# Optimization experiments

Hardware: AMD Instinct MI355X
Metric: run time of the kernel (lower is better)

The kernel has to match this reference:

```python
import jax, jax.numpy as jnp
import numpy as np

B, S, D, H = 16, 512, 1024, 16
DK = D // H
DFF = 4 * D
EPS = 1e-5
NEG = -1e9


def fake_quant(w):
    # EMA int8 symmetric per-tensor fake quantization of weights (inference view)
    scale = jnp.max(jnp.abs(w)) / 127.0
    wq = jnp.round(w / scale) * scale
    # straight-through estimator form (no-op in fwd)
    return w + jax.lax.stop_gradient(wq - w)


def layer_norm(x, g, b):
    mu = jnp.mean(x, axis=-1, keepdims=True)
    var = jnp.mean(jnp.square(x - mu), axis=-1, keepdims=True)
    return (x - mu) * jax.lax.rsqrt(var + EPS) * g + b


def setup_inputs() -> dict:
    key = jax.random.key(0)
    ks = jax.random.split(key, 16)
    std = 0.02
    inp = {
        'x': jax.random.normal(ks[0], (B, S, D), jnp.float32),
        'mask': jax.random.randint(ks[1], (B, 1, S, S), 0, 2, jnp.int32),
        'wq': jax.random.normal(ks[2], (D, D), jnp.float32) * std,
        'bq': jnp.zeros((D,), jnp.float32),
        'wk': jax.random.normal(ks[3], (D, D), jnp.float32) * std,
        'bk': jnp.zeros((D,), jnp.float32),
        'wv': jax.random.normal(ks[4], (D, D), jnp.float32) * std,
        'bv': jnp.zeros((D,), jnp.float32),
        'wo': jax.random.normal(ks[5], (D, D), jnp.float32) * std,
        'bo': jnp.zeros((D,), jnp.float32),
        'w1': jax.random.normal(ks[6], (D, DFF), jnp.float32) * std,
        'b1': jnp.zeros((DFF,), jnp.float32),
        'w2': jax.random.normal(ks[7], (DFF, D), jnp.float32) * std,
        'b2': jnp.zeros((D,), jnp.float32),
        'ln1_g': jnp.ones((D,), jnp.float32),
        'ln1_b': jnp.zeros((D,), jnp.float32),
        'ln2_g': jnp.ones((D,), jnp.float32),
        'ln2_b': jnp.zeros((D,), jnp.float32),
        'layer': 0,
    }
    return inp


def reference(x, mask, wq, bq, wk, bk, wv, bv, wo, bo, w1, b1, w2, b2,
              ln1_g, ln1_b, ln2_g, ln2_b, layer):
    # --- input sublayer: x + attention(LN(x)) (dropout = identity at eval) ---
    h = layer_norm(x, ln1_g, ln1_b)
    q = (h @ fake_quant(wq) + bq).reshape(B, S, H, DK).transpose(0, 2, 1, 3)
    k = (h @ fake_quant(wk) + bk).reshape(B, S, H, DK).transpose(0, 2, 1, 3)
    v = (h @ fake_quant(wv) + bv).reshape(B, S, H, DK).transpose(0, 2, 1, 3)
    scores = jnp.einsum('bhqd,bhkd->bhqk', q, k) * (1.0 / np.sqrt(DK))
    scores = jnp.where(mask == 0, NEG, scores)
    p = jax.nn.softmax(scores, axis=-1)
    attn = jnp.einsum('bhqk,bhkd->bhqd', p, v)
    attn = attn.transpose(0, 2, 1, 3).reshape(B, S, D)
    x = x + (attn @ wo + bo)
    # --- output sublayer: x + FFN(LN(x)), gelu (exact), middle_drop=False ---
    h2 = layer_norm(x, ln2_g, ln2_b)
    ff = jax.nn.gelu(h2 @ w1 + b1, approximate=False) @ w2 + b2
    return x + ff
```

## Files before the change

kernel.cpp:

```cpp
#include <hip/hip_runtime.h>
#include <hip/hip_bf16.h>
#include <math.h>

#define B_   16
#define S_   512
#define D_   1024
#define H_   16
#define DK_  64
#define DFF_ 4096
#define NROW (B_ * S_)
#define NEG_ (-1.0e9f)
#define SCQ_ 0.18033688011112042f

typedef __attribute__((ext_vector_type(8))) short short8v;
typedef __attribute__((ext_vector_type(4))) float f32x4;

__device__ __forceinline__ void load_lds16(const void* g, void* l) {
    __builtin_amdgcn_global_load_lds(
        reinterpret_cast<const __attribute__((address_space(1))) unsigned int*>(
            reinterpret_cast<uintptr_t>(g)),
        reinterpret_cast<__attribute__((address_space(3))) unsigned int*>(
            reinterpret_cast<uintptr_t>(l)),
        16, 0, 0);
}

__device__ __forceinline__ ushort f2bf_raw(float f) {
    __hip_bfloat16 h = __float2bfloat16(f);
    return *(ushort*)&h;
}

__device__ __forceinline__ float gelu_f(float v) {
    return 0.5f * v * (1.0f + erff(v * 0.70710678118654752f));
}

__global__ void zero_scales_k(unsigned int* p) {
    if (threadIdx.x < 3) p[threadIdx.x] = 0u;
}

__global__ void maxabs_k(const float* __restrict__ w, unsigned int* __restrict__ out, int n) {
    float m = 0.f;
    for (int i = blockIdx.x * blockDim.x + threadIdx.x; i < n; i += gridDim.x * blockDim.x)
        m = fmaxf(m, fabsf(w[i]));
#pragma unroll
    for (int off = 1; off < 64; off <<= 1)
        m = fmaxf(m, __shfl_xor(m, off));
    __shared__ float red[4];
    const int wave = threadIdx.x >> 6;
    if ((threadIdx.x & 63) == 0) red[wave] = m;
    __syncthreads();
    if (threadIdx.x == 0) {
        m = fmaxf(fmaxf(red[0], red[1]), fmaxf(red[2], red[3]));
        atomicMax(out, __float_as_uint(m));
    }
}

__global__ __launch_bounds__(256) void maskpack_k(
    const int* __restrict__ mask, unsigned long long* __restrict__ bits) {
    const int g = blockIdx.x * 4 + (threadIdx.x >> 6);
    const unsigned long long bm = __ballot(mask[(size_t)g * 64 + (threadIdx.x & 63)] != 0);
    if ((threadIdx.x & 63) == 0) bits[g] = bm;
}

__global__ __launch_bounds__(256) void transq_k(
    const float* __restrict__ W, const unsigned int* __restrict__ smax,
    __hip_bfloat16* __restrict__ Wt, int K, int N)
{
    __shared__ float t[32][33];
    const int n0 = blockIdx.x * 32, k0 = blockIdx.y * 32;
    const int tx = threadIdx.x, ty = threadIdx.y;
    float scale = 1.0f;
    if (smax) scale = __uint_as_float(*smax) * (1.0f / 127.0f);
#pragma unroll
    for (int i = 0; i < 4; ++i) {
        float v = W[(size_t)(k0 + ty + 8 * i) * N + n0 + tx];
        if (smax) v = rintf(v / scale) * scale;
        t[ty + 8 * i][tx] = v;
    }
    __syncthreads();
#pragma unroll
    for (int i = 0; i < 4; ++i)
        Wt[(size_t)(n0 + ty + 8 * i) * K + k0 + tx] = __float2bfloat16(t[tx][ty + 8 * i]);
}

__global__ __launch_bounds__(256) void ln_bf16_k(
    const float* __restrict__ x, const float* __restrict__ g,
    const float* __restrict__ b, __hip_bfloat16* __restrict__ y)
{
    const int row = blockIdx.x;
    const int tid = threadIdx.x;
    const float4 v = *(const float4*)&x[(size_t)row * D_ + tid * 4];

    float s = v.x + v.y + v.z + v.w;
#pragma unroll
    for (int off = 1; off < 64; off <<= 1) s += __shfl_xor(s, off);
    __shared__ float red[8];
    const int wave = tid >> 6, lane = tid & 63;
    if (lane == 0) red[wave] = s;
    __syncthreads();
    s = red[0] + red[1] + red[2] + red[3];
    const float mu = s * (1.0f / (float)D_);

    const float d0 = v.x - mu, d1 = v.y - mu, d2 = v.z - mu, d3 = v.w - mu;
    float sq = d0 * d0 + d1 * d1 + d2 * d2 + d3 * d3;
#pragma unroll
    for (int off = 1; off < 64; off <<= 1) sq += __shfl_xor(sq, off);
    if (lane == 0) red[4 + wave] = sq;
    __syncthreads();
    sq = red[4] + red[5] + red[6] + red[7];
    const float rs = 1.0f / sqrtf(sq * (1.0f / (float)D_) + 1e-5f);

    const float4 gv = *(const float4*)&g[tid * 4];
    const float4 bv = *(const float4*)&b[tid * 4];
    union { ushort4 u4; ushort u[4]; } cv;
    cv.u[0] = f2bf_raw(d0 * rs * gv.x + bv.x);
    cv.u[1] = f2bf_raw(d1 * rs * gv.y + bv.y);
    cv.u[2] = f2bf_raw(d2 * rs * gv.z + bv.z);
    cv.u[3] = f2bf_raw(d3 * rs * gv.w + bv.w);
    *(ushort4*)&y[(size_t)row * D_ + tid * 4] = cv.u4;
}

template <int BNT, int EPI>
__global__ __launch_bounds__(512, 2) void gemm256(
    const __hip_bfloat16* __restrict__ A, const __hip_bfloat16* __restrict__ Bt,
    const float* __restrict__ bias, const float* __restrict__ bias2,
    const float* __restrict__ bias3, const float* __restrict__ res,
    void* __restrict__ C, void* __restrict__ C2, void* __restrict__ C3,
    int M, int N, int K)
{
    constexpr int BN   = BNT * 64;
    constexpr int ABYT = 256 * 128;
    constexpr int BBYT = BN * 128;
    constexpr int BUF  = ABYT + BBYT;
    constexpr int SB   = BNT / 2;
    __shared__ __align__(16) char smem[2 * BUF];

    const int tid = threadIdx.x;
    const int w = tid >> 6, lane = tid & 63;
    const int llo = lane & 15, lhi = lane >> 4;
    const int wr = w >> 2, wc = w & 3;

    const int nwg = gridDim.x;
    const int bid = blockIdx.x;
    const int swz = (bid & 7) * (nwg >> 3) + (bid >> 3);
    const int nby = M >> 8;
    const int by = swz % nby, bx = swz / nby;
    const int row0 = by * 256, col0 = bx * BN;

    const int cko0 = ((lhi) ^ (llo & 7)) * 16;
    const int cko1 = ((4 + lhi) ^ (llo & 7)) * 16;

    const int l3 = lane >> 3;
    const int klog8 = ((lane & 7) ^ l3) * 8;
    const int rA_base = ((w >> 1) & 3) * 16 + (w & 1) * 8 + l3;
    const int rB_ws = w * 8 + l3;

    const __hip_bfloat16* Asrc[2][2];
#pragma unroll
    for (int h = 0; h < 2; ++h)
#pragma unroll
        for (int s = 0; s < 2; ++s)
            Asrc[h][s] = A + (size_t)(row0 + s * 128 + h * 64 + rA_base) * K + klog8;
    const __hip_bfloat16* Bsrc[2][2];
#pragma unroll
    for (int h = 0; h < 2; ++h)
#pragma unroll
        for (int s = 0; s < 2; ++s)
            Bsrc[h][s] = Bt + (size_t)(col0 + h * (BN / 2) + (SB == 2 ? s * 64 : 0) + rB_ws) * K + klog8;

#define STAGE_A(bufv, hh, tt) do {                                                            \
    load_lds16(Asrc[hh][0] + (size_t)(tt) * 64, smem + (bufv) * BUF + (hh) * 16384 + w * 1024);        \
    load_lds16(Asrc[hh][1] + (size_t)(tt) * 64, smem + (bufv) * BUF + (hh) * 16384 + 8192 + w * 1024); \
} while (0)
#define STAGE_B(bufv, hh, tt) do {                                                                     \
    load_lds16(Bsrc[hh][0] + (size_t)(tt) * 64, smem + (bufv) * BUF + ABYT + (hh) * (BBYT / 2) + w * 1024); \
    if (SB == 2)                                                                                       \
        load_lds16(Bsrc[hh][1] + (size_t)(tt) * 64, smem + (bufv) * BUF + ABYT + (hh) * (BBYT / 2) + 8192 + w * 1024); \
} while (0)

    f32x4 acc[8][BNT] = {};
    const int NT = K >> 6;

    STAGE_B(0, 0, 0); STAGE_B(0, 1, 0); STAGE_A(0, 0, 0); STAGE_A(0, 1, 0);
    asm volatile("s_waitcnt vmcnt(2)");
    __builtin_amdgcn_s_barrier();

    short8v bfr[BNT][2];
    for (int t = 0; t < NT; ++t) {
        const int buf = t & 1;
        const bool more = (t + 1) < NT;
        char* const base = smem + buf * BUF;
#pragma unroll
        for (int ph = 0; ph < 4; ++ph) {
            if (ph == 0) {
#pragma unroll
                for (int n = 0; n < BNT; ++n) {
                    const int brow = wc * (BNT * 16) + n * 16 + llo;
                    bfr[n][0] = *(const short8v*)(base + ABYT + brow * 128 + cko0);
                    bfr[n][1] = *(const short8v*)(base + ABYT + brow * 128 + cko1);
                }
            }
            const int mf0 = ph * 2, mf1 = ph * 2 + 1;
            const int slot0 = (mf0 >> 2) * 128 + wr * 64 + (mf0 & 3) * 16 + llo;
            const int slot1 = (mf1 >> 2) * 128 + wr * 64 + (mf1 & 3) * 16 + llo;
            const short8v a0k0 = *(const short8v*)(base + slot0 * 128 + cko0);
            const short8v a0k1 = *(const short8v*)(base + slot0 * 128 + cko1);
            const short8v a1k0 = *(const short8v*)(base + slot1 * 128 + cko0);
            const short8v a1k1 = *(const short8v*)(base + slot1 * 128 + cko1);
            if (more) {
                if (ph == 0) STAGE_B(buf ^ 1, 0, t + 1);
                if (ph == 1) STAGE_B(buf ^ 1, 1, t + 1);
                if (ph == 2) STAGE_A(buf ^ 1, 0, t + 1);
                if (ph == 3) STAGE_A(buf ^ 1, 1, t + 1);
            }
            __builtin_amdgcn_s_barrier();
            __builtin_amdgcn_s_setprio(1);
#pragma unroll
            for (int n = 0; n < BNT; ++n) {
                acc[mf0][n] = __builtin_amdgcn_mfma_f32_16x16x32_bf16(a0k0, bfr[n][0], acc[mf0][n], 0, 0, 0);
                acc[mf0][n] = __builtin_amdgcn_mfma_f32_16x16x32_bf16(a0k1, bfr[n][1], acc[mf0][n], 0, 0, 0);
                acc[mf1][n] = __builtin_amdgcn_mfma_f32_16x16x32_bf16(a1k0, bfr[n][0], acc[mf1][n], 0, 0, 0);
                acc[mf1][n] = __builtin_amdgcn_mfma_f32_16x16x32_bf16(a1k1, bfr[n][1], acc[mf1][n], 0, 0, 0);
            }
            __builtin_amdgcn_s_setprio(0);
            if (ph == 1) {
                if (more) { asm volatile("s_waitcnt vmcnt(%0)" :: "i"(2 * SB)); }
                else      { asm volatile("s_waitcnt vmcnt(0)"); }
            }
            if (ph == 3) { asm volatile("s_waitcnt vmcnt(2)"); }
            __builtin_amdgcn_s_barrier();
        }
    }
#undef STAGE_A
#undef STAGE_B

#pragma unroll
    for (int n = 0; n < BNT; ++n) {
        const int col = col0 + wc * (BNT * 16) + n * 16 + llo;
        if (EPI == 3) {
            const int proj = col0 >> 10;
            const int lcol = col & 1023;
            const float bs = (proj == 0 ? bias : proj == 1 ? bias2 : bias3)[lcol];
#pragma unroll
            for (int mf = 0; mf < 8; ++mf) {
                const int rbase = row0 + wr * 128 + mf * 16 + lhi * 4;
                if (proj == 2) {
                    const int bb = rbase >> 9, srow = rbase & 511;
                    const int hh = lcol >> 6, dk = lcol & 63;
                    union { ushort4 u4; ushort u[4]; } pk;
#pragma unroll
                    for (int j = 0; j < 4; ++j) pk.u[j] = f2bf_raw(acc[mf][n][j] + bs);
                    *(ushort4*)&((ushort*)C3)[(((size_t)(bb * 16 + hh) * 64 + dk) << 9) + srow] = pk.u4;
                } else {
                    __hip_bfloat16* dst = proj == 0 ? (__hip_bfloat16*)C : (__hip_bfloat16*)C2;
                    const float sc = proj == 0 ? SCQ_ : 1.0f;
#pragma unroll
                    for (int j = 0; j < 4; ++j)
                        dst[(size_t)(rbase + j) * D_ + lcol] = __float2bfloat16((acc[mf][n][j] + bs) * sc);
                }
            }
        } else {
            const float bs = bias[col];
#pragma unroll
            for (int mf = 0; mf < 8; ++mf) {
                const int rbase = row0 + wr * 128 + mf * 16 + lhi * 4;
#pragma unroll
                for (int j = 0; j < 4; ++j) {
                    float v = acc[mf][n][j] + bs;
                    if (EPI == 1) v = gelu_f(v);
                    if (EPI == 2) v += res[(size_t)(rbase + j) * N + col];
                    if (EPI == 1) ((__hip_bfloat16*)C)[(size_t)(rbase + j) * N + col] = __float2bfloat16(v);
                    else          ((float*)C)[(size_t)(rbase + j) * N + col] = v;
                }
            }
        }
    }
}

__global__ __launch_bounds__(256) void attn_mfma_k(
    const __hip_bfloat16* __restrict__ q, const __hip_bfloat16* __restrict__ k,
    const __hip_bfloat16* __restrict__ vt, const unsigned long long* __restrict__ mbits,
    __hip_bfloat16* __restrict__ o)
{
    const int qt = blockIdx.x;
    const int bh = blockIdx.y;
    const int b = bh >> 4, h = bh & 15;

    __shared__ __align__(16) __hip_bfloat16 Qs[64 * 72];
    __shared__ __align__(16) __hip_bfloat16 Ks[64 * 72];
    __shared__ __align__(16) __hip_bfloat16 Vts[64 * 72];
    __shared__ __align__(16) __hip_bfloat16 Pt[64 * 72];

    const int tid = threadIdx.x;
    const int w = tid >> 6, l = tid & 63;
    const int llo = l & 15, lhi = l >> 4;
    const int srow = tid >> 2, schk = tid & 3;

    {
        const __hip_bfloat16* qg =
            q + (size_t)(b * S_ + qt * 64 + srow) * D_ + h * 64 + schk * 16;
        *(short8v*)&Qs[srow * 72 + schk * 16] = *(const short8v*)qg;
        *(short8v*)&Qs[srow * 72 + schk * 16 + 8] = *(const short8v*)(qg + 8);
    }

    const __hip_bfloat16* kptr = k + (size_t)(b * S_ + srow) * D_ + h * 64 + schk * 16;
    const __hip_bfloat16* vptr = vt + (((size_t)(b * 16 + h) * 64 + srow) << 9) + schk * 16;
    short8v kr0 = *(const short8v*)kptr;
    short8v kr1 = *(const short8v*)(kptr + 8);
    short8v vr0 = *(const short8v*)vptr;
    short8v vr1 = *(const short8v*)(vptr + 8);

    __syncthreads();

    const short8v qa0 = *(const short8v*)&Qs[(w * 16 + llo) * 72 + lhi * 8];
    const short8v qa1 = *(const short8v*)&Qs[(w * 16 + llo) * 72 + 32 + lhi * 8];

    const unsigned long long* mrow =
        mbits + (((size_t)(b * S_ + qt * 64 + w * 16 + lhi * 4)) << 3);

    f32x4 oacc[4] = {};
    float m_r[4] = {-INFINITY, -INFINITY, -INFINITY, -INFINITY};
    float l_r[4] = {0.f, 0.f, 0.f, 0.f};

    for (int kt = 0; kt < 8; ++kt) {
        *(short8v*)&Ks[srow * 72 + schk * 16] = kr0;
        *(short8v*)&Ks[srow * 72 + schk * 16 + 8] = kr1;
        *(short8v*)&Vts[srow * 72 + schk * 16] = vr0;
        *(short8v*)&Vts[srow * 72 + schk * 16 + 8] = vr1;
        __syncthreads();

        short8v nk0, nk1, nv0, nv1;
        if (kt < 7) {
            const __hip_bfloat16* kp = kptr + (size_t)(kt + 1) * (64 * D_);
            const __hip_bfloat16* vp = vptr + (kt + 1) * 64;
            nk0 = *(const short8v*)kp;
            nk1 = *(const short8v*)(kp + 8);
            nv0 = *(const short8v*)vp;
            nv1 = *(const short8v*)(vp + 8);
        }

        f32x4 sacc[4] = {};
#pragma unroll
        for (int n = 0; n < 4; ++n)
            sacc[n] = __builtin_amdgcn_mfma_f32_16x16x32_bf16(
                qa0, *(const short8v*)&Ks[(n * 16 + llo) * 72 + lhi * 8], sacc[n], 0, 0, 0);
#pragma unroll
        for (int n = 0; n < 4; ++n)
            sacc[n] = __builtin_amdgcn_mfma_f32_16x16x32_bf16(
                qa1, *(const short8v*)&Ks[(n * 16 + llo) * 72 + 32 + lhi * 8], sacc[n], 0, 0, 0);

#pragma unroll
        for (int j = 0; j < 4; ++j) {
            const unsigned long long mb = mrow[j * 8 + kt];
            const float s0 = ((mb >> llo) & 1ull)        ? sacc[0][j] : NEG_;
            const float s1 = ((mb >> (llo + 16)) & 1ull) ? sacc[1][j] : NEG_;
            const float s2 = ((mb >> (llo + 32)) & 1ull) ? sacc[2][j] : NEG_;
            const float s3 = ((mb >> (llo + 48)) & 1ull) ? sacc[3][j] : NEG_;
            float pm = fmaxf(fmaxf(s0, s1), fmaxf(s2, s3));
            pm = fmaxf(pm, __shfl_xor(pm, 1));
            pm = fmaxf(pm, __shfl_xor(pm, 2));
            pm = fmaxf(pm, __shfl_xor(pm, 4));
            pm = fmaxf(pm, __shfl_xor(pm, 8));
            const float mnew = fmaxf(m_r[j], pm);
            const float alpha = exp2f(m_r[j] - mnew);
            const float p0 = exp2f(s0 - mnew);
            const float p1 = exp2f(s1 - mnew);
            const float p2 = exp2f(s2 - mnew);
            const float p3 = exp2f(s3 - mnew);
            float rsum = p0 + p1 + p2 + p3;
            rsum += __shfl_xor(rsum, 1);
            rsum += __shfl_xor(rsum, 2);
            rsum += __shfl_xor(rsum, 4);
            rsum += __shfl_xor(rsum, 8);
            l_r[j] = l_r[j] * alpha + rsum;
            m_r[j] = mnew;
#pragma unroll
            for (int df = 0; df < 4; ++df) oacc[df][j] *= alpha;
            const int prow = (w * 16 + lhi * 4 + j) * 72;
            Pt[prow + llo]      = __float2bfloat16(p0);
            Pt[prow + llo + 16] = __float2bfloat16(p1);
            Pt[prow + llo + 32] = __float2bfloat16(p2);
            Pt[prow + llo + 48] = __float2bfloat16(p3);
        }

#pragma unroll
        for (int ks = 0; ks < 2; ++ks) {
            const short8v pa = *(const short8v*)&Pt[(w * 16 + llo) * 72 + ks * 32 + lhi * 8];
#pragma unroll
            for (int df = 0; df < 4; ++df) {
                const short8v vb = *(const short8v*)&Vts[(df * 16 + llo) * 72 + ks * 32 + lhi * 8];
                oacc[df] = __builtin_amdgcn_mfma_f32_16x16x32_bf16(pa, vb, oacc[df], 0, 0, 0);
            }
        }
        __syncthreads();

        if (kt < 7) { kr0 = nk0; kr1 = nk1; vr0 = nv0; vr1 = nv1; }
    }

#pragma unroll
    for (int j = 0; j < 4; ++j) {
        const float inv = 1.0f / l_r[j];
        __hip_bfloat16* orow =
            o + (size_t)(b * S_ + qt * 64 + w * 16 + lhi * 4 + j) * D_ + h * 64;
#pragma unroll
        for (int df = 0; df < 4; ++df)
            orow[df * 16 + llo] = __float2bfloat16(oacc[df][j] * inv);
    }
}

extern "C" void kernel_launch(void* const* d_in, const int* in_sizes, int n_in,
                              void* d_out, int out_size, void* d_ws, size_t ws_size,
                              hipStream_t stream)
{
    const float* x    = (const float*)d_in[0];
    const int*   mask = (const int*)d_in[1];
    const float* wq   = (const float*)d_in[2];
    const float* bq   = (const float*)d_in[3];
    const float* wk   = (const float*)d_in[4];
    const float* bk   = (const float*)d_in[5];
    const float* wv   = (const float*)d_in[6];
    const float* bv   = (const float*)d_in[7];
    const float* wo   = (const float*)d_in[8];
    const float* bo   = (const float*)d_in[9];
    const float* w1   = (const float*)d_in[10];
    const float* b1   = (const float*)d_in[11];
    const float* w2   = (const float*)d_in[12];
    const float* b2   = (const float*)d_in[13];
    const float* ln1g = (const float*)d_in[14];
    const float* ln1b = (const float*)d_in[15];
    const float* ln2g = (const float*)d_in[16];
    const float* ln2b = (const float*)d_in[17];
    float* out = (float*)d_out;
    char* ws = (char*)d_ws;

    const size_t MB = 1024 * 1024;
    __hip_bfloat16* hb    = (__hip_bfloat16*)(ws);
    __hip_bfloat16* qbh   = (__hip_bfloat16*)(ws + 16 * MB);
    __hip_bfloat16* kbh   = (__hip_bfloat16*)(ws + 32 * MB);
    __hip_bfloat16* vth   = (__hip_bfloat16*)(ws + 48 * MB);
    __hip_bfloat16* attnb = (__hip_bfloat16*)(ws + 64 * MB);
    __hip_bfloat16* ff1b  = (__hip_bfloat16*)(ws + 16 * MB);
    __hip_bfloat16* wcat  = (__hip_bfloat16*)(ws + 80 * MB);
    __hip_bfloat16* fqqt  = (__hip_bfloat16*)(ws + 80 * MB);
    __hip_bfloat16* fqkt  = (__hip_bfloat16*)(ws + 82 * MB);
    __hip_bfloat16* fqvt  = (__hip_bfloat16*)(ws + 84 * MB);
    __hip_bfloat16* wot   = (__hip_bfloat16*)(ws + 86 * MB);
    __hip_bfloat16* w1t   = (__hip_bfloat16*)(ws + 88 * MB);
    __hip_bfloat16* w2t   = (__hip_bfloat16*)(ws + 96 * MB);
    unsigned int*   scales = (unsigned int*)(ws + 104 * MB);
    unsigned long long* mbits = (unsigned long long*)(ws + 105 * MB);

    const int NW = D_ * D_;

    zero_scales_k<<<1, 64, 0, stream>>>(scales);
    maxabs_k<<<256, 256, 0, stream>>>(wq, scales + 0, NW);
    maxabs_k<<<256, 256, 0, stream>>>(wk, scales + 1, NW);
    maxabs_k<<<256, 256, 0, stream>>>(wv, scales + 2, NW);
    maskpack_k<<<(B_ * S_ * (S_ / 64)) / 4, 256, 0, stream>>>(mask, mbits);

    const dim3 tb(32, 8);
    transq_k<<<dim3(D_ / 32, D_ / 32), tb, 0, stream>>>(wq, scales + 0, fqqt, D_, D_);
    transq_k<<<dim3(D_ / 32, D_ / 32), tb, 0, stream>>>(wk, scales + 1, fqkt, D_, D_);
    transq_k<<<dim3(D_ / 32, D_ / 32), tb, 0, stream>>>(wv, scales + 2, fqvt, D_, D_);
    transq_k<<<dim3(D_ / 32, D_ / 32), tb, 0, stream>>>(wo, nullptr, wot, D_, D_);
    transq_k<<<dim3(DFF_ / 32, D_ / 32), tb, 0, stream>>>(w1, nullptr, w1t, D_, DFF_);
    transq_k<<<dim3(D_ / 32, DFF_ / 32), tb, 0, stream>>>(w2, nullptr, w2t, DFF_, D_);

    ln_bf16_k<<<NROW, 256, 0, stream>>>(x, ln1g, ln1b, hb);

    gemm256<4, 3><<<(3 * D_ / 256) * (NROW / 256), 512, 0, stream>>>(
        hb, wcat, bq, bk, bv, nullptr, qbh, kbh, vth, NROW, 3 * D_, D_);

    attn_mfma_k<<<dim3(S_ / 64, B_ * H_), 256, 0, stream>>>(qbh, kbh, vth, mbits, attnb);

    gemm256<2, 2><<<(D_ / 128) * (NROW / 256), 512, 0, stream>>>(
        attnb, wot, bo, nullptr, nullptr, x, out, nullptr, nullptr, NROW, D_, D_);

    ln_bf16_k<<<NROW, 256, 0, stream>>>(out, ln2g, ln2b, hb);

    gemm256<4, 1><<<(DFF_ / 256) * (NROW / 256), 512, 0, stream>>>(
        hb, w1t, b1, nullptr, nullptr, nullptr, ff1b, nullptr, nullptr, NROW, DFF_, D_);

    gemm256<2, 2><<<(D_ / 128) * (NROW / 256), 512, 0, stream>>>(
        ff1b, w2t, b2, nullptr, nullptr, out, out, nullptr, nullptr, NROW, D_, DFF_);
}
```

Baseline: 474.6 us.

## Stage GEMM epilogue through LDS for vectorized stores and reorder prefetch issue

The non-QKV GEMM epilogues (GELU to bf16, and bias plus residual to fp32) now write each wave's accumulator fragment into a per-wave LDS slab. Each lane then reads back contiguous row segments and issues 16-byte vector loads of bias and residual and 16-byte vector stores, instead of scattered scalar stores per accumulator element. This targets poorly coalesced global writes in the epilogue. Separately, the main loop issues all next-tile prefetches in phases 0 and 1 and waits for them with a single vmcnt(0) at phase 3, replacing the staggered per-phase issue and partial waits. That makes memory traffic burstier and may reduce overlap slack.

Measured after the change: 452.9 us. 4.6% less time.

```diff
diff --git a/kernel.cpp b/kernel.cpp
--- a/kernel.cpp
+++ b/kernel.cpp
@@ -181,7 +181,7 @@
     const int NT = K >> 6;
 
     STAGE_B(0, 0, 0); STAGE_B(0, 1, 0); STAGE_A(0, 0, 0); STAGE_A(0, 1, 0);
-    asm volatile("s_waitcnt vmcnt(2)");
+    asm volatile("s_waitcnt vmcnt(0)");
     __builtin_amdgcn_s_barrier();
 
     short8v bfr[BNT][2];
@@ -207,10 +207,8 @@
             const short8v a1k0 = *(const short8v*)(base + slot1 * 128 + cko0);
             const short8v a1k1 = *(const short8v*)(base + slot1 * 128 + cko1);
             if (more) {
-                if (ph == 0) STAGE_B(buf ^ 1, 0, t + 1);
-                if (ph == 1) STAGE_B(buf ^ 1, 1, t + 1);
-                if (ph == 2) STAGE_A(buf ^ 1, 0, t + 1);
-                if (ph == 3) STAGE_A(buf ^ 1, 1, t + 1);
+                if (ph == 0) { STAGE_B(buf ^ 1, 0, t + 1); STAGE_B(buf ^ 1, 1, t + 1); }
+                else if (ph == 1) { STAGE_A(buf ^ 1, 0, t + 1); STAGE_A(buf ^ 1, 1, t + 1); }
             }
             __builtin_amdgcn_s_barrier();
             __builtin_amdgcn_s_setprio(1);
@@ -222,21 +220,17 @@
                 acc[mf1][n] = __builtin_amdgcn_mfma_f32_16x16x32_bf16(a1k1, bfr[n][1], acc[mf1][n], 0, 0, 0);
             }
             __builtin_amdgcn_s_setprio(0);
-            if (ph == 1) {
-                if (more) { asm volatile("s_waitcnt vmcnt(%0)" :: "i"(2 * SB)); }
-                else      { asm volatile("s_waitcnt vmcnt(0)"); }
-            }
-            if (ph == 3) { asm volatile("s_waitcnt vmcnt(2)"); }
+            if (ph == 3) { asm volatile("s_waitcnt vmcnt(0)"); }
             __builtin_amdgcn_s_barrier();
         }
     }
 #undef STAGE_A
 #undef STAGE_B
 
-#pragma unroll
-    for (int n = 0; n < BNT; ++n) {
-        const int col = col0 + wc * (BNT * 16) + n * 16 + llo;
-        if (EPI == 3) {
+    if (EPI == 3) {
+#pragma unroll
+        for (int n = 0; n < BNT; ++n) {
+            const int col = col0 + wc * (BNT * 16) + n * 16 + llo;
             const int proj = col0 >> 10;
             const int lcol = col & 1023;
             const float bs = (proj == 0 ? bias : proj == 1 ? bias2 : bias3)[lcol];
@@ -258,18 +252,49 @@
                         dst[(size_t)(rbase + j) * D_ + lcol] = __float2bfloat16((acc[mf][n][j] + bs) * sc);
                 }
             }
-        } else {
-            const float bs = bias[col];
-#pragma unroll
-            for (int mf = 0; mf < 8; ++mf) {
-                const int rbase = row0 + wr * 128 + mf * 16 + lhi * 4;
-#pragma unroll
-                for (int j = 0; j < 4; ++j) {
-                    float v = acc[mf][n][j] + bs;
-                    if (EPI == 1) v = gelu_f(v);
-                    if (EPI == 2) v += res[(size_t)(rbase + j) * N + col];
-                    if (EPI == 1) ((__hip_bfloat16*)C)[(size_t)(rbase + j) * N + col] = __float2bfloat16(v);
-                    else          ((float*)C)[(size_t)(rbase + j) * N + col] = v;
+        }
+    } else {
+        constexpr int WCOL = BNT * 16;
+        constexpr int ESTR = WCOL + 4;
+        float* const eslab = (float*)smem + w * (16 * ESTR);
+        const int rr = lane >> 2;
+        const int cq = lane & 3;
+        const int c0 = cq * (BNT * 4);
+        const int gcolb = col0 + wc * WCOL + c0;
+#pragma unroll
+        for (int mf = 0; mf < 8; ++mf) {
+#pragma unroll
+            for (int n = 0; n < BNT; ++n)
+#pragma unroll
+                for (int j = 0; j < 4; ++j)
+                    eslab[(lhi * 4 + j) * ESTR + n * 16 + llo] = acc[mf][n][j];
+            const int grow = row0 + wr * 128 + mf * 16 + rr;
+            if (EPI == 1) {
+                ushort tmp[BNT * 4];
+#pragma unroll
+                for (int i = 0; i < BNT; ++i) {
+                    float4 v = *(float4*)&eslab[rr * ESTR + c0 + i * 4];
+                    const float4 b4 = *(const float4*)&bias[gcolb + i * 4];
+                    tmp[i * 4 + 0] = f2bf_raw(gelu_f(v.x + b4.x));
+                    tmp[i * 4 + 1] = f2bf_raw(gelu_f(v.y + b4.y));
+                    tmp[i * 4 + 2] = f2bf_raw(gelu_f(v.z + b4.z));
+                    tmp[i * 4 + 3] = f2bf_raw(gelu_f(v.w + b4.w));
+                }
+                ushort* dst = (ushort*)C + (size_t)grow * N + gcolb;
+#pragma unroll
+                for (int i = 0; i < BNT / 2; ++i)
+                    *(short8v*)(dst + i * 8) = *(short8v*)&tmp[i * 8];
+            } else {
+#pragma unroll
+                for (int i = 0; i < BNT; ++i) {
+                    float4 v = *(float4*)&eslab[rr * ESTR + c0 + i * 4];
+                    const float4 b4 = *(const float4*)&bias[gcolb + i * 4];
+                    const float4 r4 = *(const float4*)&res[(size_t)grow * N + gcolb + i * 4];
+                    v.x += b4.x + r4.x;
+                    v.y += b4.y + r4.y;
+                    v.z += b4.z + r4.z;
+                    v.w += b4.w + r4.w;
+                    *(float4*)&((float*)C)[(size_t)grow * N + gcolb + i * 4] = v;
                 }
             }
         }
```
